# Kernel optimization log

Hardware: AMD Instinct MI355X
Metric: run time of the kernel (lower is better)

The kernel has to match this reference:

```python
import jax, jax.numpy as jnp
import numpy as np

C1 = 512
RATIO = 16


def setup_inputs() -> dict:
    key = jax.random.key(0)
    k1, k2, k3 = jax.random.split(key, 3)
    x = jax.random.normal(k1, (32, C1, 64, 64), dtype=jnp.float32)
    # Linear(c1, c1//ratio, bias=False): weight shape (out, in)
    w1 = jax.random.normal(k2, (C1 // RATIO, C1), dtype=jnp.float32) * (1.0 / np.sqrt(C1))
    w2 = jax.random.normal(k3, (C1, C1 // RATIO), dtype=jnp.float32) * (1.0 / np.sqrt(C1 // RATIO))
    return {"x": x, "w1": w1, "w2": w2}


def reference(x, w1, w2):
    b, c, h, w = x.shape
    # squeeze: global avg pool -> (b, c)
    y = jnp.mean(x, axis=(2, 3))
    # excitation MLP: Linear -> ReLU -> Linear -> Sigmoid
    y = jax.nn.relu(jnp.einsum('bc,rc->br', y, w1))
    y = jax.nn.sigmoid(jnp.einsum('br,cr->bc', y, w2))
    # top half channels by gate value (torch.sort descending + slice == top_k)
    half_ch = c // 2
    y_half, indices = jax.lax.top_k(y, half_ch)  # (b, half_ch)
    # per-sample channel gather, then scale by the gate
    x_half = jnp.take_along_axis(x, indices[:, :, None, None], axis=1)  # (b, half_ch, h, w)
    return x_half * y_half[:, :, None, None]
```

## Files before the change

kernel.cpp:

```cpp
#include <hip/hip_runtime.h>
#include <math.h>

#define B   32
#define C   512
#define R   32
#define HW  4096
#define HALF 256

__global__ __launch_bounds__(256) void se_mean_kernel(const float* __restrict__ x,
                                                      float* __restrict__ means) {
    const int bc = blockIdx.x;
    const float4* xp = (const float4*)(x + (size_t)bc * HW);
    const int t = threadIdx.x;
    float s = 0.f;
#pragma unroll
    for (int i = 0; i < 4; ++i) {
        float4 v = xp[t + i * 256];
        s += (v.x + v.y) + (v.z + v.w);
    }
#pragma unroll
    for (int off = 32; off > 0; off >>= 1) s += __shfl_down(s, off, 64);
    __shared__ float wsum[4];
    const int lane = t & 63, wid = t >> 6;
    if (lane == 0) wsum[wid] = s;
    __syncthreads();
    if (t == 0) {
        means[bc] = (wsum[0] + wsum[1] + wsum[2] + wsum[3]) * (1.0f / HW);
    }
}

__global__ __launch_bounds__(512) void se_gate_topk_kernel(const float* __restrict__ means,
                                                           const float* __restrict__ w1,
                                                           const float* __restrict__ w2,
                                                           int* __restrict__ idx_out,
                                                           float* __restrict__ gate_out) {
    const int b = blockIdx.x;
    const int t = threadIdx.x;
    __shared__ float sm[C];
    __shared__ float sy1[R];
    __shared__ float sy2[C];

    sm[t] = means[b * C + t];
    __syncthreads();

    if (t < R) {
        float acc = 0.f;
        for (int c = 0; c < C; ++c) acc += sm[c] * w1[t * C + c];
        sy1[t] = fmaxf(acc, 0.f);
    }
    __syncthreads();

    {
        float acc = 0.f;
#pragma unroll
        for (int r = 0; r < R; ++r) acc += sy1[r] * w2[t * R + r];
        sy2[t] = 1.0f / (1.0f + expf(-acc));
    }
    __syncthreads();

    const float v = sy2[t];
    int rank = 0;
    for (int j = 0; j < C; ++j) {
        float u = sy2[j];
        rank += (u > v) || (u == v && j < t);
    }
    if (rank < HALF) {
        idx_out[b * HALF + rank]  = t;
        gate_out[b * HALF + rank] = v;
    }
}

__global__ __launch_bounds__(256) void se_gather_scale_kernel(const float* __restrict__ x,
                                                              const int* __restrict__ idx,
                                                              const float* __restrict__ gate,
                                                              float* __restrict__ out) {
    const int bk = blockIdx.x;
    const int b  = bk >> 8;
    const int ch = idx[bk];
    const float g = gate[bk];
    const float4* src = (const float4*)(x + ((size_t)b * C + ch) * HW);
    float4* dst = (float4*)(out + (size_t)bk * HW);
    const int t = threadIdx.x;
#pragma unroll
    for (int i = 0; i < 4; ++i) {
        float4 v = src[t + i * 256];
        v.x *= g; v.y *= g; v.z *= g; v.w *= g;
        dst[t + i * 256] = v;
    }
}

extern "C" void kernel_launch(void* const* d_in, const int* in_sizes, int n_in,
                              void* d_out, int out_size, void* d_ws, size_t ws_size,
                              hipStream_t stream) {
    const float* x  = (const float*)d_in[0];
    const float* w1 = (const float*)d_in[1];
    const float* w2 = (const float*)d_in[2];
    float* out = (float*)d_out;

    float* means = (float*)d_ws;
    int*   idx   = (int*)((char*)d_ws + B * C * 4);
    float* gate  = (float*)((char*)d_ws + B * C * 4 + B * HALF * 4);

    se_mean_kernel<<<B * C, 256, 0, stream>>>(x, means);
    se_gate_topk_kernel<<<B, 512, 0, stream>>>(means, w1, w2, idx, gate);
    se_gather_scale_kernel<<<B * HALF, 256, 0, stream>>>(x, idx, gate, out);
}
```

Baseline: 445.4 us.

## Use one wavefront per row, nontemporal stores, and parallelize gate MLP

The mean and gather kernels now give each 64-lane wavefront a whole channel row, with 16 float4 loads in flight per lane. This removes the shared-memory/syncthreads reduction and raises memory-level parallelism. The gather kernel writes output with nontemporal stores so the large output does not pollute cache. The gate kernel splits the first linear layer across all 512 threads with partial sums, and vectorizes the rank-based top-k scan with float4 LDS reads. The cost is higher register use per thread and fewer, larger blocks.

Measured after the change: 435.8 us. -2.2%, faster.

```diff
diff --git a/kernel.cpp b/kernel.cpp
--- a/kernel.cpp
+++ b/kernel.cpp
@@ -1,32 +1,30 @@
 #include <hip/hip_runtime.h>
 #include <math.h>
 
-#define B   32
-#define C   512
-#define R   32
-#define HW  4096
+#define B    32
+#define C    512
+#define R    32
+#define HW   4096
 #define HALF 256
 
 __global__ __launch_bounds__(256) void se_mean_kernel(const float* __restrict__ x,
                                                       float* __restrict__ means) {
-    const int bc = blockIdx.x;
-    const float4* xp = (const float4*)(x + (size_t)bc * HW);
-    const int t = threadIdx.x;
+    const int t    = threadIdx.x;
+    const int lane = t & 63;
+    const int wid  = t >> 6;
+    const int row  = blockIdx.x * 4 + wid;
+    const float4* xp = (const float4*)(x + (size_t)row * HW);
+
+    float4 v[16];
+#pragma unroll
+    for (int i = 0; i < 16; ++i) v[i] = xp[lane + 64 * i];
     float s = 0.f;
 #pragma unroll
-    for (int i = 0; i < 4; ++i) {
-        float4 v = xp[t + i * 256];
-        s += (v.x + v.y) + (v.z + v.w);
-    }
+    for (int i = 0; i < 16; ++i) s += (v[i].x + v[i].y) + (v[i].z + v[i].w);
+
 #pragma unroll
     for (int off = 32; off > 0; off >>= 1) s += __shfl_down(s, off, 64);
-    __shared__ float wsum[4];
-    const int lane = t & 63, wid = t >> 6;
-    if (lane == 0) wsum[wid] = s;
-    __syncthreads();
-    if (t == 0) {
-        means[bc] = (wsum[0] + wsum[1] + wsum[2] + wsum[3]) * (1.0f / HW);
-    }
+    if (lane == 0) means[row] = s * (1.0f / HW);
 }
 
 __global__ __launch_bounds__(512) void se_gate_topk_kernel(const float* __restrict__ means,
@@ -37,15 +35,27 @@
     const int b = blockIdx.x;
     const int t = threadIdx.x;
     __shared__ float sm[C];
+    __shared__ float ps[R][17];
     __shared__ float sy1[R];
     __shared__ float sy2[C];
 
     sm[t] = means[b * C + t];
     __syncthreads();
 
+    {
+        const int r   = t & 31;
+        const int seg = t >> 5;
+        const int c0  = seg * 32;
+        float acc = 0.f;
+#pragma unroll
+        for (int i = 0; i < 32; ++i) acc += sm[c0 + i] * w1[r * C + c0 + i];
+        ps[r][seg] = acc;
+    }
+    __syncthreads();
     if (t < R) {
         float acc = 0.f;
-        for (int c = 0; c < C; ++c) acc += sm[c] * w1[t * C + c];
+#pragma unroll
+        for (int s = 0; s < 16; ++s) acc += ps[t][s];
         sy1[t] = fmaxf(acc, 0.f);
     }
     __syncthreads();
@@ -59,10 +69,16 @@
     __syncthreads();
 
     const float v = sy2[t];
+    const float4* sv = (const float4*)sy2;
     int rank = 0;
-    for (int j = 0; j < C; ++j) {
-        float u = sy2[j];
-        rank += (u > v) || (u == v && j < t);
+#pragma unroll 4
+    for (int j4 = 0; j4 < C / 4; ++j4) {
+        float4 u = sv[j4];
+        const int j = j4 * 4;
+        rank += (u.x > v) || (u.x == v && (j + 0) < t);
+        rank += (u.y > v) || (u.y == v && (j + 1) < t);
+        rank += (u.z > v) || (u.z == v && (j + 2) < t);
+        rank += (u.w > v) || (u.w == v && (j + 3) < t);
     }
     if (rank < HALF) {
         idx_out[b * HALF + rank]  = t;
@@ -74,18 +90,24 @@
                                                               const int* __restrict__ idx,
                                                               const float* __restrict__ gate,
                                                               float* __restrict__ out) {
-    const int bk = blockIdx.x;
-    const int b  = bk >> 8;
-    const int ch = idx[bk];
-    const float g = gate[bk];
+    const int t    = threadIdx.x;
+    const int lane = t & 63;
+    const int wid  = t >> 6;
+    const int bk   = blockIdx.x * 4 + wid;
+    const int b    = bk >> 8;
+    const int ch   = idx[bk];
+    const float g  = gate[bk];
     const float4* src = (const float4*)(x + ((size_t)b * C + ch) * HW);
     float4* dst = (float4*)(out + (size_t)bk * HW);
-    const int t = threadIdx.x;
+
 #pragma unroll
-    for (int i = 0; i < 4; ++i) {
-        float4 v = src[t + i * 256];
+    for (int i = 0; i < 16; ++i) {
+        float4 v = src[lane + 64 * i];
         v.x *= g; v.y *= g; v.z *= g; v.w *= g;
-        dst[t + i * 256] = v;
+        __builtin_nontemporal_store(v.x, &dst[lane + 64 * i].x);
+        __builtin_nontemporal_store(v.y, &dst[lane + 64 * i].y);
+        __builtin_nontemporal_store(v.z, &dst[lane + 64 * i].z);
+        __builtin_nontemporal_store(v.w, &dst[lane + 64 * i].w);
     }
 }
 
@@ -101,7 +123,7 @@
     int*   idx   = (int*)((char*)d_ws + B * C * 4);
     float* gate  = (float*)((char*)d_ws + B * C * 4 + B * HALF * 4);
 
-    se_mean_kernel<<<B * C, 256, 0, stream>>>(x, means);
+    se_mean_kernel<<<B * C / 4, 256, 0, stream>>>(x, means);
     se_gate_topk_kernel<<<B, 512, 0, stream>>>(means, w1, w2, idx, gate);
-    se_gather_scale_kernel<<<B * HALF, 256, 0, stream>>>(x, idx, gate, out);
+    se_gather_scale_kernel<<<B * HALF / 4, 256, 0, stream>>>(x, idx, gate, out);
 }
```
